# Kernel tuning notes

Measured on AMD Instinct MI355X. Metric: run time of the kernel, lower is better.

## Reference

```python
import jax, jax.numpy as jnp
import numpy as np

EPS = 0.01
BETA = 0.8
GAMMA_A = 0.01
GAMMA_W = 0.01
ALPHA = 1.0
N_UNITS = 128

def setup_inputs() -> dict:
    key = jax.random.key(0)
    ks = jax.random.split(key, 7)
    B, T, D_in, C_out = 512, 1024, 64, 10
    return {
        "x": jax.random.normal(ks[0], (B, T, D_in), dtype=jnp.float32),
        "E_w": jax.random.normal(ks[1], (N_UNITS, D_in), dtype=jnp.float32) / np.sqrt(D_in),
        "E_b": jax.random.normal(ks[2], (N_UNITS,), dtype=jnp.float32) * 0.01,
        "B_p": jax.random.normal(ks[3], (N_UNITS, N_UNITS), dtype=jnp.float32) / N_UNITS,
        "C_p": jax.random.normal(ks[4], (N_UNITS, N_UNITS), dtype=jnp.float32) / N_UNITS,
        "D_w": jax.random.normal(ks[5], (C_out, N_UNITS), dtype=jnp.float32) / np.sqrt(N_UNITS),
        "D_b": jax.random.normal(ks[6], (C_out,), dtype=jnp.float32) * 0.01,
    }

def reference(x, E_w, E_b, B_p, C_p, D_w, D_b):
    B, T, _ = x.shape
    I = jnp.eye(N_UNITS, dtype=x.dtype)
    # Skew/symmetric mixture recurrent matrices (computed once, as in i==0 branch)
    A = BETA * (B_p - B_p.T) + (1.0 - BETA) * (B_p + B_p.T) - GAMMA_A * I
    W = BETA * (C_p - C_p.T) + (1.0 - BETA) * (C_p + C_p.T) - GAMMA_W * I
    # Input projection for all timesteps at once: [T, B, n_units]
    Z = jnp.einsum('bti,ui->tbu', x, E_w) + E_b
    h0 = jnp.zeros((B, N_UNITS), dtype=x.dtype)

    def step(h, z):
        h_update = ALPHA * (h @ A) + jnp.tanh(h @ W + z)
        return h + EPS * h_update, None

    h_final, _ = jax.lax.scan(step, h0, Z)
    return h_final @ D_w.T + D_b
```

## Files before the change

kernel.cpp:

```cpp
#include <hip/hip_runtime.h>

#define EPS_C 0.01f
#define NU    128
#define DIN   64
#define COUT  10

typedef float    f32x4 __attribute__((ext_vector_type(4)));
typedef _Float16 f16x4 __attribute__((ext_vector_type(4)));
typedef _Float16 f16x8 __attribute__((ext_vector_type(8)));

#define MFMA32(A, B, C) __builtin_amdgcn_mfma_f32_16x16x32_f16((A), (B), (C), 0, 0, 0)
#define BAR() asm volatile("s_waitcnt lgkmcnt(0)\n\ts_barrier" ::: "memory")

__global__ __launch_bounds__(512, 1)
void rnn_core(const float* __restrict__ x,
              const float* __restrict__ E_w, const float* __restrict__ E_b,
              const float* __restrict__ B_p, const float* __restrict__ C_p,
              const float* __restrict__ D_w, const float* __restrict__ D_b,
              float* __restrict__ out, int T)
{
    const int tid  = threadIdx.x;
    const int lane = tid & 63;
    const int w    = tid >> 6;
    const int lid  = lane & 15;
    const int q    = lane >> 4;
    const int g    = blockIdx.x;

    __shared__ _Float16 xs[2][16 * 2 * 64 * 8];
    __shared__ _Float16 hbuf[2][4][64][8];
    __shared__ float    hfin[16][NU + 4];

    f16x8 AT[4], WT[4], EF[2];
    f32x4 ebv;
    {
        const int m = w * 16 + lid;
        #pragma unroll
        for (int kt = 0; kt < 4; ++kt) {
            f16x8 fa, fw;
            #pragma unroll
            for (int j = 0; j < 8; ++j) {
                const int k  = kt * 32 + q * 8 + j;
                const float dg = (k == m) ? 0.01f : 0.0f;
                fa[j] = (_Float16)(B_p[k * NU + m] - 0.6f * B_p[m * NU + k] - dg);
                fw[j] = (_Float16)(C_p[k * NU + m] - 0.6f * C_p[m * NU + k] - dg);
            }
            AT[kt] = fa;  WT[kt] = fw;
        }
        #pragma unroll
        for (int kt = 0; kt < 2; ++kt) {
            f16x8 fe;
            #pragma unroll
            for (int j = 0; j < 8; ++j)
                fe[j] = (_Float16)E_w[m * DIN + kt * 32 + q * 8 + j];
            EF[kt] = fe;
        }
        #pragma unroll
        for (int r = 0; r < 4; ++r)
            ebv[r] = E_b[w * 16 + q * 4 + r];
    }

    const int bb = tid & 15;
    const int s2 = (tid >> 4) & 15;
    const int tp = tid >> 8;
    const float* xrow = x + ((size_t)(g * 16 + bb) * T) * DIN + s2 * 4;
    const int wb2 = (((s2 >> 3) * 64) + (((s2 >> 1) & 3) * 16) + bb) * 16 + (s2 & 1) * 8;

    float4 xg[8];

#define STAGE_WRITE(BUF)                                                      \
    {                                                                         \
        char* base_ = (char*)&xs[(BUF)][0];                                   \
        _Pragma("unroll")                                                     \
        for (int i2 = 0; i2 < 8; ++i2) {                                      \
            float4 v_ = xg[i2];                                               \
            f16x4 h4_;                                                        \
            h4_[0] = (_Float16)v_.x; h4_[1] = (_Float16)v_.y;                 \
            h4_[2] = (_Float16)v_.z; h4_[3] = (_Float16)v_.w;                 \
            *(f16x4*)(base_ + (2 * i2 + tp) * 2048 + wb2) = h4_;              \
        }                                                                     \
    }

    if (tid < 256)
        ((float4*)&hbuf[0][0][0][0])[tid] = (float4){0.f, 0.f, 0.f, 0.f};
    #pragma unroll
    for (int i = 0; i < 8; ++i)
        xg[i] = *(const float4*)(xrow + (size_t)(2 * i + tp) * DIN);
    STAGE_WRITE(0)
    __syncthreads();

    f32x4 hf = {0.f, 0.f, 0.f, 0.f};
    f32x4 zc;
    {
        f16x8 x0 = *(const f16x8*)((char*)&xs[0][0] + (0 * 64 + lane) * 16);
        f16x8 x1 = *(const f16x8*)((char*)&xs[0][0] + (1 * 64 + lane) * 16);
        zc = ebv;
        zc = MFMA32(EF[0], x0, zc);
        zc = MFMA32(EF[1], x1, zc);
    }

    const int nch = T >> 4;
    for (int c = 0; c < nch; ++c) {
        if (c + 1 < nch) {
            const float* xr2 = xrow + (size_t)(c + 1) * 16 * DIN;
            #pragma unroll
            for (int i = 0; i < 8; ++i)
                xg[i] = *(const float4*)(xr2 + (size_t)(2 * i + tp) * DIN);
        }
        #pragma unroll
        for (int i = 0; i < 16; ++i) {
            const int t  = c * 16 + i;
            const int p  = i & 1;
            const int np = p ^ 1;

            f16x8 hB[4];
            #pragma unroll
            for (int kt = 0; kt < 4; ++kt)
                hB[kt] = *(const f16x8*)((char*)&hbuf[p][0][0][0] + (kt * 64 + lane) * 16);

            int tt = t + 1; if (tt >= T) tt = T - 1;
            const int it = tt & 15;
            char* xb = (char*)&xs[(tt >> 4) & 1][0];
            f16x8 xfA = *(const f16x8*)(xb + ((it * 2 + 0) * 64 + lane) * 16);
            f16x8 xfB = *(const f16x8*)(xb + ((it * 2 + 1) * 64 + lane) * 16);

            f32x4 ya = {0.f, 0.f, 0.f, 0.f};
            f32x4 wa = zc;
            #pragma unroll
            for (int kt = 0; kt < 4; ++kt) {
                ya = MFMA32(AT[kt], hB[kt], ya);
                wa = MFMA32(WT[kt], hB[kt], wa);
            }

            {
                f16x4 nh;
                #pragma unroll
                for (int r = 0; r < 4; ++r) {
                    const float arg = wa[r];
                    const float e2  = __expf(2.0f * arg);
                    const float th  = 1.0f - 2.0f * __builtin_amdgcn_rcpf(e2 + 1.0f);
                    const float hv  = hf[r] + EPS_C * (ya[r] + th);
                    hf[r] = hv;
                    nh[r] = (_Float16)hv;
                }
                char* hwp = (char*)&hbuf[np][w >> 1][0][0];
                const int row = (2 * (w & 1) + (q >> 1)) * 16 + lid;
                *(f16x4*)(hwp + row * 16 + (q & 1) * 8) = nh;
            }

            f32x4 zn = ebv;
            zn = MFMA32(EF[0], xfA, zn);
            zn = MFMA32(EF[1], xfB, zn);
            zc = zn;

            if (i == 13 && c + 1 < nch) STAGE_WRITE((c + 1) & 1)
            BAR();
        }
    }

    #pragma unroll
    for (int r = 0; r < 4; ++r)
        hfin[lid][w * 16 + q * 4 + r] = hf[r];
    __syncthreads();

    if (tid < 16 * COUT) {
        const int r  = tid / COUT;
        const int cc = tid - r * COUT;
        float acc = D_b[cc];
        #pragma unroll 8
        for (int u = 0; u < NU; ++u)
            acc = fmaf(hfin[r][u], D_w[cc * NU + u], acc);
        out[((size_t)g * 16 + r) * COUT + cc] = acc;
    }
}

extern "C" void kernel_launch(void* const* d_in, const int* in_sizes, int n_in,
                              void* d_out, int out_size, void* d_ws, size_t ws_size,
                              hipStream_t stream)
{
    const float* x   = (const float*)d_in[0];
    const float* E_w = (const float*)d_in[1];
    const float* E_b = (const float*)d_in[2];
    const float* B_p = (const float*)d_in[3];
    const float* C_p = (const float*)d_in[4];
    const float* D_w = (const float*)d_in[5];
    const float* D_b = (const float*)d_in[6];
    float* out = (float*)d_out;

    const int B  = out_size / COUT;
    const int T  = in_sizes[0] / (B * DIN);
    const int NB = B / 16;

    rnn_core<<<NB, 512, 0, stream>>>(x, E_w, E_b, B_p, C_p, D_w, D_b, out, T);
}
```

Baseline: 598.0 us.

## Pack two 16-row batch groups per 1024-thread block and fold EPS into A

Each block now runs two independent 16-row batch groups, each on 8 waves with its own x and h buffers, so there are half as many blocks with twice the threads. The shared per-step barrier now couples both groups. EPS is folded into the A matrix and the h-update MFMAs accumulate straight into the state, which removes the separate ya accumulator and simplifies the tanh update. The x staging chunk shrinks to 8 timesteps and its conversion writes are spread across four steps instead of one. Trade-offs: EPS-scaled A in fp16 may lose some precision, and with 512 rows only 16 blocks are launched, which risks leaving CUs idle.

```diff
diff --git a/kernel.cpp b/kernel.cpp
--- a/kernel.cpp
+++ b/kernel.cpp
@@ -12,7 +12,7 @@
 #define MFMA32(A, B, C) __builtin_amdgcn_mfma_f32_16x16x32_f16((A), (B), (C), 0, 0, 0)
 #define BAR() asm volatile("s_waitcnt lgkmcnt(0)\n\ts_barrier" ::: "memory")
 
-__global__ __launch_bounds__(512, 1)
+__global__ __launch_bounds__(1024)
 void rnn_core(const float* __restrict__ x,
               const float* __restrict__ E_w, const float* __restrict__ E_b,
               const float* __restrict__ B_p, const float* __restrict__ C_p,
@@ -22,18 +22,19 @@
     const int tid  = threadIdx.x;
     const int lane = tid & 63;
     const int w    = tid >> 6;
+    const int gw   = w >> 3;
+    const int wl   = w & 7;
     const int lid  = lane & 15;
     const int q    = lane >> 4;
-    const int g    = blockIdx.x;
-
-    __shared__ _Float16 xs[2][16 * 2 * 64 * 8];
-    __shared__ _Float16 hbuf[2][4][64][8];
-    __shared__ float    hfin[16][NU + 4];
+
+    __shared__ _Float16 xs[2][2][8 * 2 * 64 * 8];
+    __shared__ _Float16 hbuf[2][2][4][64][8];
+    __shared__ float    hfin[2][16][NU + 4];
 
     f16x8 AT[4], WT[4], EF[2];
     f32x4 ebv;
     {
-        const int m = w * 16 + lid;
+        const int m = wl * 16 + lid;
         #pragma unroll
         for (int kt = 0; kt < 4; ++kt) {
             f16x8 fa, fw;
@@ -41,8 +42,10 @@
             for (int j = 0; j < 8; ++j) {
                 const int k  = kt * 32 + q * 8 + j;
                 const float dg = (k == m) ? 0.01f : 0.0f;
-                fa[j] = (_Float16)(B_p[k * NU + m] - 0.6f * B_p[m * NU + k] - dg);
-                fw[j] = (_Float16)(C_p[k * NU + m] - 0.6f * C_p[m * NU + k] - dg);
+                const float av = B_p[k * NU + m] - 0.6f * B_p[m * NU + k] - dg;
+                const float wv = C_p[k * NU + m] - 0.6f * C_p[m * NU + k] - dg;
+                fa[j] = (_Float16)(EPS_C * av);
+                fw[j] = (_Float16)wv;
             }
             AT[kt] = fa;  WT[kt] = fw;
         }
@@ -56,120 +59,130 @@
         }
         #pragma unroll
         for (int r = 0; r < 4; ++r)
-            ebv[r] = E_b[w * 16 + q * 4 + r];
-    }
-
-    const int bb = tid & 15;
-    const int s2 = (tid >> 4) & 15;
-    const int tp = tid >> 8;
-    const float* xrow = x + ((size_t)(g * 16 + bb) * T) * DIN + s2 * 4;
+            ebv[r] = E_b[wl * 16 + q * 4 + r];
+    }
+
+    const int gtid = tid & 511;
+    const int bb = gtid & 15;
+    const int s2 = (gtid >> 4) & 15;
+    const int tp = gtid >> 8;
+    const int g0 = blockIdx.x * 32 + gw * 16;
+    const float* xrow = x + ((size_t)(g0 + bb) * T) * DIN + s2 * 4;
     const int wb2 = (((s2 >> 3) * 64) + (((s2 >> 1) & 3) * 16) + bb) * 16 + (s2 & 1) * 8;
 
-    float4 xg[8];
-
-#define STAGE_WRITE(BUF)                                                      \
-    {                                                                         \
-        char* base_ = (char*)&xs[(BUF)][0];                                   \
-        _Pragma("unroll")                                                     \
-        for (int i2 = 0; i2 < 8; ++i2) {                                      \
-            float4 v_ = xg[i2];                                               \
-            f16x4 h4_;                                                        \
-            h4_[0] = (_Float16)v_.x; h4_[1] = (_Float16)v_.y;                 \
-            h4_[2] = (_Float16)v_.z; h4_[3] = (_Float16)v_.w;                 \
-            *(f16x4*)(base_ + (2 * i2 + tp) * 2048 + wb2) = h4_;              \
-        }                                                                     \
-    }
+    float4 xg[4];
 
     if (tid < 256)
-        ((float4*)&hbuf[0][0][0][0])[tid] = (float4){0.f, 0.f, 0.f, 0.f};
+        ((float4*)&hbuf[0][0][0][0][0])[tid] = (float4){0.f, 0.f, 0.f, 0.f};
+    else if (tid < 512)
+        ((float4*)&hbuf[1][0][0][0][0])[tid - 256] = (float4){0.f, 0.f, 0.f, 0.f};
     #pragma unroll
-    for (int i = 0; i < 8; ++i)
-        xg[i] = *(const float4*)(xrow + (size_t)(2 * i + tp) * DIN);
-    STAGE_WRITE(0)
+    for (int i2 = 0; i2 < 4; ++i2)
+        xg[i2] = *(const float4*)(xrow + (size_t)(2 * i2 + tp) * DIN);
+    {
+        char* base_ = (char*)&xs[gw][0][0];
+        #pragma unroll
+        for (int i2 = 0; i2 < 4; ++i2) {
+            float4 v_ = xg[i2];
+            f16x4 h4_;
+            h4_[0] = (_Float16)v_.x; h4_[1] = (_Float16)v_.y;
+            h4_[2] = (_Float16)v_.z; h4_[3] = (_Float16)v_.w;
+            *(f16x4*)(base_ + (2 * i2 + tp) * 2048 + wb2) = h4_;
+        }
+    }
     __syncthreads();
 
-    f32x4 hf = {0.f, 0.f, 0.f, 0.f};
+    f32x4 ha = {0.f, 0.f, 0.f, 0.f};
     f32x4 zc;
     {
-        f16x8 x0 = *(const f16x8*)((char*)&xs[0][0] + (0 * 64 + lane) * 16);
-        f16x8 x1 = *(const f16x8*)((char*)&xs[0][0] + (1 * 64 + lane) * 16);
+        f16x8 x0 = *(const f16x8*)((char*)&xs[gw][0][0] + (0 * 64 + lane) * 16);
+        f16x8 x1 = *(const f16x8*)((char*)&xs[gw][0][0] + (1 * 64 + lane) * 16);
         zc = ebv;
         zc = MFMA32(EF[0], x0, zc);
         zc = MFMA32(EF[1], x1, zc);
     }
 
-    const int nch = T >> 4;
+    const int nch = T >> 3;
     for (int c = 0; c < nch; ++c) {
         if (c + 1 < nch) {
-            const float* xr2 = xrow + (size_t)(c + 1) * 16 * DIN;
-            #pragma unroll
-            for (int i = 0; i < 8; ++i)
-                xg[i] = *(const float4*)(xr2 + (size_t)(2 * i + tp) * DIN);
-        }
-        #pragma unroll
-        for (int i = 0; i < 16; ++i) {
-            const int t  = c * 16 + i;
+            #pragma unroll
+            for (int i2 = 0; i2 < 4; ++i2)
+                xg[i2] = *(const float4*)(xrow + (size_t)((c + 1) * 8 + 2 * i2 + tp) * DIN);
+        }
+        #pragma unroll
+        for (int i = 0; i < 8; ++i) {
+            const int t  = c * 8 + i;
             const int p  = i & 1;
             const int np = p ^ 1;
 
             f16x8 hB[4];
             #pragma unroll
             for (int kt = 0; kt < 4; ++kt)
-                hB[kt] = *(const f16x8*)((char*)&hbuf[p][0][0][0] + (kt * 64 + lane) * 16);
+                hB[kt] = *(const f16x8*)((char*)&hbuf[gw][p][0][0][0] + (kt * 64 + lane) * 16);
 
             int tt = t + 1; if (tt >= T) tt = T - 1;
-            const int it = tt & 15;
-            char* xb = (char*)&xs[(tt >> 4) & 1][0];
+            const int it = tt & 7;
+            char* xb = (char*)&xs[gw][(tt >> 3) & 1][0];
             f16x8 xfA = *(const f16x8*)(xb + ((it * 2 + 0) * 64 + lane) * 16);
             f16x8 xfB = *(const f16x8*)(xb + ((it * 2 + 1) * 64 + lane) * 16);
 
-            f32x4 ya = {0.f, 0.f, 0.f, 0.f};
             f32x4 wa = zc;
             #pragma unroll
-            for (int kt = 0; kt < 4; ++kt) {
-                ya = MFMA32(AT[kt], hB[kt], ya);
+            for (int kt = 0; kt < 4; ++kt)
                 wa = MFMA32(WT[kt], hB[kt], wa);
-            }
+            #pragma unroll
+            for (int kt = 0; kt < 4; ++kt)
+                ha = MFMA32(AT[kt], hB[kt], ha);
 
             {
                 f16x4 nh;
                 #pragma unroll
                 for (int r = 0; r < 4; ++r) {
-                    const float arg = wa[r];
-                    const float e2  = __expf(2.0f * arg);
-                    const float th  = 1.0f - 2.0f * __builtin_amdgcn_rcpf(e2 + 1.0f);
-                    const float hv  = hf[r] + EPS_C * (ya[r] + th);
-                    hf[r] = hv;
+                    const float e2 = __expf(2.0f * wa[r]);
+                    const float rc = __builtin_amdgcn_rcpf(e2 + 1.0f);
+                    const float hv = fmaf(-2.0f * EPS_C, rc, ha[r] + EPS_C);
+                    ha[r] = hv;
                     nh[r] = (_Float16)hv;
                 }
-                char* hwp = (char*)&hbuf[np][w >> 1][0][0];
-                const int row = (2 * (w & 1) + (q >> 1)) * 16 + lid;
+                char* hwp = (char*)&hbuf[gw][np][wl >> 1][0][0];
+                const int row = (2 * (wl & 1) + (q >> 1)) * 16 + lid;
                 *(f16x4*)(hwp + row * 16 + (q & 1) * 8) = nh;
             }
 
-            f32x4 zn = ebv;
-            zn = MFMA32(EF[0], xfA, zn);
-            zn = MFMA32(EF[1], xfB, zn);
-            zc = zn;
-
-            if (i == 13 && c + 1 < nch) STAGE_WRITE((c + 1) & 1)
+            {
+                f32x4 zn = ebv;
+                zn = MFMA32(EF[0], xfA, zn);
+                zn = MFMA32(EF[1], xfB, zn);
+                zc = zn;
+            }
+
+            if (c + 1 < nch && i >= 4) {
+                const int i2 = i - 4;
+                float4 v_ = xg[i2];
+                f16x4 h4_;
+                h4_[0] = (_Float16)v_.x; h4_[1] = (_Float16)v_.y;
+                h4_[2] = (_Float16)v_.z; h4_[3] = (_Float16)v_.w;
+                *(f16x4*)((char*)&xs[gw][(c + 1) & 1][0] + (2 * i2 + tp) * 2048 + wb2) = h4_;
+            }
             BAR();
         }
     }
 
     #pragma unroll
     for (int r = 0; r < 4; ++r)
-        hfin[lid][w * 16 + q * 4 + r] = hf[r];
+        hfin[gw][lid][wl * 16 + q * 4 + r] = ha[r];
     __syncthreads();
 
-    if (tid < 16 * COUT) {
-        const int r  = tid / COUT;
-        const int cc = tid - r * COUT;
+    if (tid < 2 * 16 * COUT) {
+        const int gg  = tid / 160;
+        const int rem = tid - gg * 160;
+        const int r   = rem / COUT;
+        const int cc  = rem - r * COUT;
         float acc = D_b[cc];
         #pragma unroll 8
         for (int u = 0; u < NU; ++u)
-            acc = fmaf(hfin[r][u], D_w[cc * NU + u], acc);
-        out[((size_t)g * 16 + r) * COUT + cc] = acc;
+            acc = fmaf(hfin[gg][r][u], D_w[cc * NU + u], acc);
+        out[((size_t)(blockIdx.x * 32 + gg * 16 + r)) * COUT + cc] = acc;
     }
 }
 
@@ -188,7 +201,7 @@
 
     const int B  = out_size / COUT;
     const int T  = in_sizes[0] / (B * DIN);
-    const int NB = B / 16;
-
-    rnn_core<<<NB, 512, 0, stream>>>(x, E_w, E_b, B_p, C_p, D_w, D_b, out, T);
+    const int NB = B / 32;
+
+    rnn_core<<<NB, 1024, 0, stream>>>(x, E_w, E_b, B_p, C_p, D_w, D_b, out, T);
 }
```

Result: slower. 856.3 us (+43.2%).
